# Kernel optimization log

Measured on AMD Instinct MI355X. Metric: run time of the kernel, lower is better.

Reference implementation:

```python
import jax, jax.numpy as jnp
import numpy as np

B, S, D, H, HD = 1, 2048, 1024, 16, 64
E, K, F = 8, 2, 2048
Z_COEF, LB_COEF = 0.001, 0.01


def setup_inputs() -> dict:
    key = jax.random.key(0)
    ks = jax.random.split(key, 10)
    s_d = 1.0 / np.sqrt(D)
    s_f = 1.0 / np.sqrt(F)
    return {
        'hidden_states': jax.random.normal(ks[0], (B, S, D), jnp.float32),
        'attention_mask': jnp.tril(jnp.ones((S, S), bool))[None, None],  # causal [1,1,S,S]
        'position_ids': jnp.broadcast_to(jnp.arange(S), (B, S)),
        'ln1_w': jnp.ones((D,), jnp.float32), 'ln1_b': jnp.zeros((D,), jnp.float32),
        'ln2_w': jnp.ones((D,), jnp.float32), 'ln2_b': jnp.zeros((D,), jnp.float32),
        'wq': jax.random.normal(ks[1], (D, D), jnp.float32) * s_d,
        'wk': jax.random.normal(ks[2], (D, D), jnp.float32) * s_d,
        'wv': jax.random.normal(ks[3], (D, D), jnp.float32) * s_d,
        'wo': jax.random.normal(ks[4], (D, D), jnp.float32) * s_d,
        'w_router': jax.random.normal(ks[5], (D, E), jnp.float32) * s_d,
        'w_gate': jax.random.normal(ks[6], (E, D, F), jnp.float32) * s_d,
        'w_up': jax.random.normal(ks[7], (E, D, F), jnp.float32) * s_d,
        'w_down': jax.random.normal(ks[8], (E, F, D), jnp.float32) * s_f,
    }


def _layernorm(x, w, b):
    m = x.mean(-1, keepdims=True)
    v = jnp.mean(jnp.square(x - m), -1, keepdims=True)
    return (x - m) / jnp.sqrt(v + 1e-5) * w + b


def _rotate_half(x):
    x1, x2 = jnp.split(x, 2, axis=-1)
    return jnp.concatenate([-x2, x1], axis=-1)


def _forward(hs, mask, pos, l1w, l1b, l2w, l2b, wq, wk, wv, wo, wr, wg, wu, wd):
    b, s, d = hs.shape
    # --- attention sub-block ---
    res = hs
    x = _layernorm(hs, l1w, l1b)
    q = (x @ wq).reshape(b, s, H, HD).transpose(0, 2, 1, 3)  # [b,H,s,hd]
    k = (x @ wk).reshape(b, s, H, HD).transpose(0, 2, 1, 3)
    v = (x @ wv).reshape(b, s, H, HD).transpose(0, 2, 1, 3)
    inv_freq = 1.0 / (10000.0 ** (jnp.arange(0, HD, 2, dtype=jnp.float32) / HD))
    freqs = pos[..., None].astype(jnp.float32) * inv_freq  # [b,s,hd/2]
    cos = jnp.cos(freqs); sin = jnp.sin(freqs)
    cos = jnp.concatenate([cos, cos], -1)[:, None]  # [b,1,s,hd]
    sin = jnp.concatenate([sin, sin], -1)[:, None]
    q = q * cos + _rotate_half(q) * sin
    k = k * cos + _rotate_half(k) * sin
    scores = jnp.einsum('bhqd,bhkd->bhqk', q, k) / np.sqrt(HD)
    scores = jnp.where(mask, scores, jnp.asarray(-1e9, scores.dtype))
    attn_w = jax.nn.softmax(scores, axis=-1)
    a = jnp.einsum('bhqk,bhkd->bhqd', attn_w, v)
    a = a.transpose(0, 2, 1, 3).reshape(b, s, d)
    hs = res + a @ wo
    # --- MoE sub-block ---
    res = hs
    x = _layernorm(hs, l2w, l2b)
    xt = x.reshape(-1, d)  # [T,D]
    logits = xt @ wr  # [T,E]
    probs = jax.nn.softmax(logits.astype(jnp.float32), axis=-1)
    ew, ei = jax.lax.top_k(probs, K)  # [T,K]
    ew = ew / ew.sum(-1, keepdims=True)
    one_hot = jax.nn.one_hot(ei, E, dtype=jnp.float32)  # [T,K,E]
    combine = jnp.sum(one_hot * ew[..., None], axis=1).astype(xt.dtype)  # [T,E]
    g = jnp.einsum('td,edf->etf', xt, wg)
    u = jnp.einsum('td,edf->etf', xt, wu)
    y = jnp.einsum('etf,efd->etd', jax.nn.silu(g) * u, wd)  # [E,T,D]
    moe_out = jnp.einsum('te,etd->td', combine, y).reshape(b, s, d)
    # --- aux losses ---
    z_loss = Z_COEF * jnp.mean(jnp.square(jax.scipy.special.logsumexp(logits, axis=-1)))
    expert_mask = jnp.sum(one_hot, axis=1)  # [T,E] in {0,1}
    util = expert_mask.sum(0) / (b * s)
    lb_loss = LB_COEF * jnp.sum(util * probs.mean(0))
    aux = z_loss + lb_loss
    return res + moe_out, aux


def reference(hidden_states, attention_mask, position_ids, ln1_w, ln1_b, ln2_w, ln2_b,
              wq, wk, wv, wo, w_router, w_gate, w_up, w_down):
    return _forward(hidden_states, attention_mask, position_ids, ln1_w, ln1_b, ln2_w, ln2_b,
                    wq, wk, wv, wo, w_router, w_gate, w_up, w_down)
```

## Files before the change

kernel.cpp:

```cpp
#include <hip/hip_runtime.h>
#include <math.h>

static constexpr int S = 2048;
static constexpr int D = 1024;
static constexpr int H = 16;
static constexpr int HD = 64;
static constexpr int E = 8;
static constexpr int F = 2048;
static constexpr int NSLOTS = S * 2;
static constexpr int NPAD = NSLOTS + 128;

typedef __attribute__((ext_vector_type(8))) short bf16x8;
typedef __attribute__((ext_vector_type(4))) float f32x4;

__device__ __forceinline__ float bf2f(ushort u) {
    uint32_t x = ((uint32_t)u) << 16; float f; __builtin_memcpy(&f, &x, 4); return f;
}
__device__ __forceinline__ ushort f2bf(float f) {
    uint32_t x; __builtin_memcpy(&x, &f, 4);
    return (ushort)((x + 0x7fffu + ((x >> 16) & 1u)) >> 16);
}
__device__ __forceinline__ void async_copy16(const void* gptr, void* ldsptr) {
    __builtin_amdgcn_global_load_lds(
        (const __attribute__((address_space(1))) void*)gptr,
        (__attribute__((address_space(3))) void*)ldsptr, 16, 0, 0);
}

__global__ __launch_bounds__(256) void castT_kernel(const float* __restrict__ src,
    ushort* __restrict__ dst, int K, int N)
{
    __shared__ float T[64][65];
    int z = blockIdx.z;
    src += (size_t)z * K * N; dst += (size_t)z * K * N;
    int k0 = blockIdx.y * 64, n0 = blockIdx.x * 64;
    int t = threadIdx.x;
    int r = t >> 4, c4 = (t & 15) * 4;
#pragma unroll
    for (int it = 0; it < 4; it++) {
        float4 v = *(const float4*)(src + (size_t)(k0 + r + it * 16) * N + n0 + c4);
        T[r + it * 16][c4 + 0] = v.x; T[r + it * 16][c4 + 1] = v.y;
        T[r + it * 16][c4 + 2] = v.z; T[r + it * 16][c4 + 3] = v.w;
    }
    __syncthreads();
#pragma unroll
    for (int it = 0; it < 4; it++) {
        int rr = r + it * 16;
        ushort4 o;
        o.x = f2bf(T[c4 + 0][rr]); o.y = f2bf(T[c4 + 1][rr]);
        o.z = f2bf(T[c4 + 2][rr]); o.w = f2bf(T[c4 + 3][rr]);
        *(ushort4*)(dst + (size_t)(n0 + rr) * K + k0 + c4) = o;
    }
}

__global__ __launch_bounds__(256) void castT2_kernel(const float* __restrict__ src,
    ushort* __restrict__ dh, ushort* __restrict__ dl, int K, int N)
{
    __shared__ float T[64][65];
    src += (size_t)blockIdx.z * K * N;
    dh += (size_t)blockIdx.z * K * N; dl += (size_t)blockIdx.z * K * N;
    int k0 = blockIdx.y * 64, n0 = blockIdx.x * 64;
    int t = threadIdx.x;
    int r = t >> 4, c4 = (t & 15) * 4;
#pragma unroll
    for (int it = 0; it < 4; it++) {
        float4 v = *(const float4*)(src + (size_t)(k0 + r + it * 16) * N + n0 + c4);
        T[r + it * 16][c4 + 0] = v.x; T[r + it * 16][c4 + 1] = v.y;
        T[r + it * 16][c4 + 2] = v.z; T[r + it * 16][c4 + 3] = v.w;
    }
    __syncthreads();
#pragma unroll
    for (int it = 0; it < 4; it++) {
        int rr = r + it * 16;
        ushort4 oh, ol;
        float v0 = T[c4 + 0][rr], v1 = T[c4 + 1][rr], v2 = T[c4 + 2][rr], v3 = T[c4 + 3][rr];
        oh.x = f2bf(v0); ol.x = f2bf(v0 - bf2f(oh.x));
        oh.y = f2bf(v1); ol.y = f2bf(v1 - bf2f(oh.y));
        oh.z = f2bf(v2); ol.z = f2bf(v2 - bf2f(oh.z));
        oh.w = f2bf(v3); ol.w = f2bf(v3 - bf2f(oh.w));
        *(ushort4*)(dh + (size_t)(n0 + rr) * K + k0 + c4) = oh;
        *(ushort4*)(dl + (size_t)(n0 + rr) * K + k0 + c4) = ol;
    }
}

__global__ __launch_bounds__(256) void ln_kernel(const float* __restrict__ x,
    const float* __restrict__ w, const float* __restrict__ b,
    float* __restrict__ yf, ushort* __restrict__ yh, ushort* __restrict__ yl)
{
    int t = blockIdx.x, tid = threadIdx.x;
    __shared__ float redx[256];
    __shared__ float redy[256];
    const float* xr = x + (size_t)t * D;
    float4 xv = *(const float4*)(xr + tid * 4);
    redx[tid] = xv.x + xv.y + xv.z + xv.w;
    redy[tid] = xv.x * xv.x + xv.y * xv.y + xv.z * xv.z + xv.w * xv.w;
    __syncthreads();
    for (int st = 128; st > 0; st >>= 1) {
        if (tid < st) { redx[tid] += redx[tid + st]; redy[tid] += redy[tid + st]; }
        __syncthreads();
    }
    float mean = redx[0] * (1.0f / D);
    float var  = redy[0] * (1.0f / D) - mean * mean;
    float rstd = rsqrtf(var + 1e-5f);
    float4 wv = *(const float4*)(w + tid * 4);
    float4 bv = *(const float4*)(b + tid * 4);
    float4 o;
    o.x = (xv.x - mean) * rstd * wv.x + bv.x;
    o.y = (xv.y - mean) * rstd * wv.y + bv.y;
    o.z = (xv.z - mean) * rstd * wv.z + bv.z;
    o.w = (xv.w - mean) * rstd * wv.w + bv.w;
    if (yf) *(float4*)(yf + (size_t)t * D + tid * 4) = o;
    ushort4 oh;
    oh.x = f2bf(o.x); oh.y = f2bf(o.y); oh.z = f2bf(o.z); oh.w = f2bf(o.w);
    if (yh) *(ushort4*)(yh + (size_t)t * D + tid * 4) = oh;
    if (yl) {
        ushort4 ol;
        ol.x = f2bf(o.x - bf2f(oh.x)); ol.y = f2bf(o.y - bf2f(oh.y));
        ol.z = f2bf(o.z - bf2f(oh.z)); ol.w = f2bf(o.w - bf2f(oh.w));
        *(ushort4*)(yl + (size_t)t * D + tid * 4) = ol;
    }
}

__global__ __launch_bounds__(512) void rope_cast(const float* __restrict__ q,
    const float* __restrict__ k, ushort* __restrict__ qh, ushort* __restrict__ ql,
    ushort* __restrict__ kh, ushort* __restrict__ kl)
{
    int t = blockIdx.x;
    int idx = threadIdx.x;
    int hh = idx >> 5, i = idx & 31;
    float invf = powf(10000.0f, -(float)i / 32.0f);
    float ang = (float)t * invf;
    float cc = cosf(ang), ss = sinf(ang);
    size_t base = (size_t)t * D + hh * HD + i;
    const float QS = 0.125f * 1.4426950408889634f;
    float q1 = q[base], q2 = q[base + 32];
    float qr1 = (q1 * cc - q2 * ss) * QS;
    float qr2 = (q2 * cc + q1 * ss) * QS;
    ushort h1 = f2bf(qr1); qh[base] = h1;      ql[base] = f2bf(qr1 - bf2f(h1));
    ushort h2 = f2bf(qr2); qh[base + 32] = h2; ql[base + 32] = f2bf(qr2 - bf2f(h2));
    float k1 = k[base], k2 = k[base + 32];
    float kr1 = k1 * cc - k2 * ss;
    float kr2 = k2 * cc + k1 * ss;
    ushort h3 = f2bf(kr1); kh[base] = h3;      kl[base] = f2bf(kr1 - bf2f(h3));
    ushort h4 = f2bf(kr2); kh[base + 32] = h4; kl[base + 32] = f2bf(kr2 - bf2f(h4));
}

__device__ __forceinline__ void stage_m2(const ushort* __restrict__ Ah_g,
    const ushort* __restrict__ Al_g, const ushort* __restrict__ Bh_g,
    const ushort* __restrict__ Bl_g, int lda, int ldb, int kbase,
    ushort* sAh, ushort* sAl, ushort* sBh, ushort* sBl, int tid, int w)
{
    {
        int ckc = tid >> 6, r = tid & 63;
        int loff = (w * 64) * 8;
        size_t ga = (size_t)r * lda + kbase + ckc * 8;
        async_copy16(Ah_g + ga, sAh + loff);
        async_copy16(Al_g + ga, sAl + loff);
    }
#pragma unroll
    for (int it = 0; it < 2; it++) {
        int c = it * 256 + tid;
        int ckc = c >> 7, r = c & 127;
        int loff = (it * 256 + w * 64) * 8;
        size_t gb = (size_t)r * ldb + kbase + ckc * 8;
        async_copy16(Bh_g + gb, sBh + loff);
        async_copy16(Bl_g + gb, sBl + loff);
    }
}

__device__ __forceinline__ void mfma2_kloop(const ushort* __restrict__ Ah_g,
    const ushort* __restrict__ Al_g, const ushort* __restrict__ Bh_g,
    const ushort* __restrict__ Bl_g, int lda, int ldb, int K,
    ushort (&sAh)[2][2048], ushort (&sAl)[2][2048],
    ushort (&sBh)[2][4096], ushort (&sBl)[2][4096], f32x4 (&acc)[2][4])
{
    const int tid = threadIdx.x;
    const int w = tid >> 6, l = tid & 63;
    const int wm = (w >> 1) * 32, wn = (w & 1) * 64;
    const int kc = l >> 4, lr = l & 15;
    const int NT = K / 32;
    stage_m2(Ah_g, Al_g, Bh_g, Bl_g, lda, ldb, 0, sAh[0], sAl[0], sBh[0], sBl[0], tid, w);
    for (int t = 0; t < NT; ++t) {
        const int cur = t & 1;
        asm volatile("s_waitcnt vmcnt(0)" ::: "memory");
        __builtin_amdgcn_s_barrier();
        __builtin_amdgcn_sched_barrier(0);
        if (t + 1 < NT)
            stage_m2(Ah_g, Al_g, Bh_g, Bl_g, lda, ldb, (t + 1) * 32,
                     sAh[1 - cur], sAl[1 - cur], sBh[1 - cur], sBl[1 - cur], tid, w);
        bf16x8 ah[2], al[2], bh[4], bl[4];
#pragma unroll
        for (int f = 0; f < 2; f++) {
            int ao = (kc * 64 + wm + f * 16 + lr) * 8;
            ah[f] = *(const bf16x8*)(sAh[cur] + ao);
            al[f] = *(const bf16x8*)(sAl[cur] + ao);
        }
#pragma unroll
        for (int f = 0; f < 4; f++) {
            int bo = (kc * 128 + wn + f * 16 + lr) * 8;
            bh[f] = *(const bf16x8*)(sBh[cur] + bo);
            bl[f] = *(const bf16x8*)(sBl[cur] + bo);
        }
#pragma unroll
        for (int fm = 0; fm < 2; fm++)
#pragma unroll
            for (int fn = 0; fn < 4; fn++) {
                acc[fm][fn] = __builtin_amdgcn_mfma_f32_16x16x32_bf16(ah[fm], bh[fn], acc[fm][fn], 0, 0, 0);
                acc[fm][fn] = __builtin_amdgcn_mfma_f32_16x16x32_bf16(ah[fm], bl[fn], acc[fm][fn], 0, 0, 0);
                acc[fm][fn] = __builtin_amdgcn_mfma_f32_16x16x32_bf16(al[fm], bh[fn], acc[fm][fn], 0, 0, 0);
            }
    }
}

__global__ __launch_bounds__(256) void qkv_mfma2(const ushort* __restrict__ xh,
    const ushort* __restrict__ xl,
    const ushort* __restrict__ wqh, const ushort* __restrict__ wql,
    const ushort* __restrict__ wkh, const ushort* __restrict__ wkl,
    const ushort* __restrict__ wvh, const ushort* __restrict__ wvl,
    float* __restrict__ qo, float* __restrict__ ko, float* __restrict__ vo)
{
    __shared__ ushort sAh[2][2048], sAl[2][2048], sBh[2][4096], sBl[2][4096];
    const ushort* Bh = blockIdx.z == 0 ? wqh : (blockIdx.z == 1 ? wkh : wvh);
    const ushort* Bl = blockIdx.z == 0 ? wql : (blockIdx.z == 1 ? wkl : wvl);
    float* C = blockIdx.z == 0 ? qo : (blockIdx.z == 1 ? ko : vo);
    int m0 = blockIdx.y * 64, n0 = blockIdx.x * 128;
    f32x4 acc[2][4];
#pragma unroll
    for (int i = 0; i < 2; i++)
#pragma unroll
        for (int j = 0; j < 4; j++) acc[i][j] = (f32x4){0.f, 0.f, 0.f, 0.f};
    mfma2_kloop(xh + (size_t)m0 * D, xl + (size_t)m0 * D,
                Bh + (size_t)n0 * D, Bl + (size_t)n0 * D, D, D, D,
                sAh, sAl, sBh, sBl, acc);
    const int l = threadIdx.x & 63, w = threadIdx.x >> 6;
    const int wm = (w >> 1) * 32, wn = (w & 1) * 64;
#pragma unroll
    for (int fm = 0; fm < 2; fm++)
#pragma unroll
        for (int fn = 0; fn < 4; fn++)
#pragma unroll
            for (int r = 0; r < 4; r++) {
                int row = m0 + wm + fm * 16 + (l >> 4) * 4 + r;
                int col = n0 + wn + fn * 16 + (l & 15);
                C[(size_t)row * D + col] = acc[fm][fn][r];
            }
}

__global__ __launch_bounds__(256) void wo_mfma2(const ushort* __restrict__ ah,
    const ushort* __restrict__ al, const ushort* __restrict__ wh, const ushort* __restrict__ wl,
    const float* __restrict__ resid, float* __restrict__ Cout)
{
    __shared__ ushort sAh[2][2048], sAl[2][2048], sBh[2][4096], sBl[2][4096];
    int m0 = blockIdx.y * 64, n0 = blockIdx.x * 128;
    f32x4 acc[2][4];
#pragma unroll
    for (int i = 0; i < 2; i++)
#pragma unroll
        for (int j = 0; j < 4; j++) acc[i][j] = (f32x4){0.f, 0.f, 0.f, 0.f};
    mfma2_kloop(ah + (size_t)m0 * D, al + (size_t)m0 * D,
                wh + (size_t)n0 * D, wl + (size_t)n0 * D, D, D, D,
                sAh, sAl, sBh, sBl, acc);
    const int l = threadIdx.x & 63, w = threadIdx.x >> 6;
    const int wm = (w >> 1) * 32, wn = (w & 1) * 64;
#pragma unroll
    for (int fm = 0; fm < 2; fm++)
#pragma unroll
        for (int fn = 0; fn < 4; fn++)
#pragma unroll
            for (int r = 0; r < 4; r++) {
                int row = m0 + wm + fm * 16 + (l >> 4) * 4 + r;
                int col = n0 + wn + fn * 16 + (l & 15);
                Cout[(size_t)row * D + col] = acc[fm][fn][r] + resid[(size_t)row * D + col];
            }
}

__global__ __launch_bounds__(256) void attn_mfma(
    const ushort* __restrict__ qhp, const ushort* __restrict__ qlp,
    const ushort* __restrict__ khp, const ushort* __restrict__ klp,
    const ushort* __restrict__ vth, const ushort* __restrict__ vtl,
    ushort* __restrict__ oh_out, ushort* __restrict__ ol_out)
{
    __shared__ ushort sK[2][2][4096];
    __shared__ ushort sV[2][2][4096];
    __shared__ ushort sP[4][2][1024];
    const int n = blockIdx.y * 32 + blockIdx.x;
    const int wg = ((n & 7) << 6) + (n >> 3);
    const int h = wg >> 5;
    const int qt = 31 - (wg & 31);
    const int tid = threadIdx.x;
    const int w = tid >> 6, l = tid & 63;
    const int g = l >> 4, c = l & 15;
    const size_t hoff = (size_t)h * HD;
    ushort* sPh = &sP[w][0][0];
    ushort* sPl = &sP[w][1][0];

#define STAGE_KV(buf, kt_)                                                        \
  do {                                                                            \
    const int k0s = (kt_) * 64;                                                   \
    int cb0 = w * 64;                                                             \
    int ch0 = cb0 + l;                                                            \
    size_t kg0 = (size_t)(k0s + (ch0 & 63)) * D + hoff + (ch0 >> 6) * 8;          \
    size_t vg0 = (hoff + (ch0 & 63)) * (size_t)S + k0s + (ch0 >> 6) * 8;          \
    async_copy16(khp + kg0, &sK[buf][0][cb0 * 8]);                                \
    async_copy16(klp + kg0, &sK[buf][1][cb0 * 8]);                                \
    async_copy16(vth + vg0, &sV[buf][0][cb0 * 8]);                                \
    async_copy16(vtl + vg0, &sV[buf][1][cb0 * 8]);                                \
    int cb1 = 256 + w * 64;                                                       \
    int ch1 = cb1 + l;                                                            \
    size_t kg1 = (size_t)(k0s + (ch1 & 63)) * D + hoff + (ch1 >> 6) * 8;          \
    size_t vg1 = (hoff + (ch1 & 63)) * (size_t)S + k0s + (ch1 >> 6) * 8;          \
    async_copy16(khp + kg1, &sK[buf][0][cb1 * 8]);                                \
    async_copy16(klp + kg1, &sK[buf][1][cb1 * 8]);                                \
    async_copy16(vth + vg1, &sV[buf][0][cb1 * 8]);                                \
// ... 90 lines not shown
        }
        const ushort* sVh = &sV[cur][0][0];
        const ushort* sVl = &sV[cur][1][0];
        bf16x8 pa0 = *(const bf16x8*)(sPh + (g * 16 + c) * 8);
        bf16x8 pa1 = *(const bf16x8*)(sPh + ((4 + g) * 16 + c) * 8);
        bf16x8 pb0 = *(const bf16x8*)(sPl + (g * 16 + c) * 8);
        bf16x8 pb1 = *(const bf16x8*)(sPl + ((4 + g) * 16 + c) * 8);
#pragma unroll
        for (int fn = 0; fn < 4; fn++) {
            int u0 = (g * 64 + fn * 16 + c) * 8;
            int u1 = ((4 + g) * 64 + fn * 16 + c) * 8;
            bf16x8 vh0 = *(const bf16x8*)(sVh + u0);
            bf16x8 vh1 = *(const bf16x8*)(sVh + u1);
            bf16x8 vl0 = *(const bf16x8*)(sVl + u0);
            bf16x8 vl1 = *(const bf16x8*)(sVl + u1);
            f32x4 o = oacc[fn];
            o = __builtin_amdgcn_mfma_f32_16x16x32_bf16(pa0, vh0, o, 0, 0, 0);
            o = __builtin_amdgcn_mfma_f32_16x16x32_bf16(pa1, vh1, o, 0, 0, 0);
            o = __builtin_amdgcn_mfma_f32_16x16x32_bf16(pa0, vl0, o, 0, 0, 0);
            o = __builtin_amdgcn_mfma_f32_16x16x32_bf16(pa1, vl1, o, 0, 0, 0);
            o = __builtin_amdgcn_mfma_f32_16x16x32_bf16(pb0, vh0, o, 0, 0, 0);
            o = __builtin_amdgcn_mfma_f32_16x16x32_bf16(pb1, vh1, o, 0, 0, 0);
            oacc[fn] = o;
        }
        if (kt < qt) {
            asm volatile("s_waitcnt vmcnt(0)" ::: "memory");
            __builtin_amdgcn_s_barrier();
            __builtin_amdgcn_sched_barrier(0);
        }
    }
#pragma unroll
    for (int r = 0; r < 4; r++) {
        float inv = 1.0f / l_[r];
        size_t orow = (size_t)(qt * 64 + w * 16 + g * 4 + r) * D + hoff;
#pragma unroll
        for (int fn = 0; fn < 4; fn++) {
            float v = oacc[fn][r] * inv;
            ushort hi = f2bf(v);
            oh_out[orow + fn * 16 + c] = hi;
            ol_out[orow + fn * 16 + c] = f2bf(v - bf2f(hi));
        }
    }
#undef STAGE_KV
}

__global__ __launch_bounds__(64) void router_kernel(const float* __restrict__ x,
    const float* __restrict__ wr, int* __restrict__ ei, float* __restrict__ ew,
    int* __restrict__ counts, float* __restrict__ prob_sums, float* __restrict__ z_sum)
{
    int t = blockIdx.x, lane = threadIdx.x;
    const float* xr = x + (size_t)t * D;
    float p[E] = {};
    for (int d = lane; d < D; d += 64) {
        float xd = xr[d];
        const float* wrow = wr + d * E;
#pragma unroll
        for (int e = 0; e < E; e++) p[e] = fmaf(xd, wrow[e], p[e]);
    }
#pragma unroll
    for (int off = 32; off > 0; off >>= 1) {
#pragma unroll
        for (int e = 0; e < E; e++) p[e] += __shfl_xor(p[e], off);
    }
    float m = p[0];
#pragma unroll
    for (int e = 1; e < E; e++) m = fmaxf(m, p[e]);
    float sum = 0.0f, pr[E];
#pragma unroll
    for (int e = 0; e < E; e++) { pr[e] = expf(p[e] - m); sum += pr[e]; }
    float invs = 1.0f / sum;
#pragma unroll
    for (int e = 0; e < E; e++) pr[e] *= invs;
    float lse = m + logf(sum);
// ... 20 lines not shown
    if (tid < E) { counts[tid] = 0; prob_sums[tid] = 0.0f; }
    if (tid == 0) *z_sum = 0.0f;
}

__global__ void finalize_kernel(const int* __restrict__ counts, const float* __restrict__ prob_sums,
    const float* __restrict__ z_sum, int* __restrict__ offs, int* __restrict__ cursor,
    float* __restrict__ aux_out)
{
    if (threadIdx.x == 0) {
        int off = 0;
        for (int e = 0; e < E; e++) { offs[e] = off; cursor[e] = off; off += counts[e]; }
        float z = 1e-3f * (*z_sum) * (1.0f / S);
        float lb = 0.0f;
        for (int e = 0; e < E; e++) lb += ((float)counts[e] / (float)S) * (prob_sums[e] / (float)S);
        lb *= 1e-2f;
        *aux_out = z + lb;
    }
}

__global__ __launch_bounds__(256) void scatter_kernel(const int* __restrict__ ei,
    int* __restrict__ cursor, int* __restrict__ tlist, int* __restrict__ slot_of)
{
    int t = blockIdx.x * 256 + threadIdx.x;
    if (t >= S) return;
#pragma unroll
    for (int kk = 0; kk < 2; kk++) {
        int e = ei[2 * t + kk];
        int slot = atomicAdd(&cursor[e], 1);
        tlist[slot] = t;
        slot_of[2 * t + kk] = slot;
    }
}

__global__ __launch_bounds__(256) void gather_kernel(const ushort* __restrict__ xbf,
    const int* __restrict__ tlist, ushort* __restrict__ xg)
{
    int slot = blockIdx.x;
    int t4 = threadIdx.x * 4;
    ushort4 vv;
    if (slot < NSLOTS) {
        int tok = tlist[slot];
        vv = *(const ushort4*)(xbf + (size_t)tok * D + t4);
    } else {
        vv = make_ushort4(0, 0, 0, 0);
    }
    *(ushort4*)(xg + (size_t)slot * D + t4) = vv;
}

__global__ __launch_bounds__(256) void moe_gateup_mfma(const ushort* __restrict__ xg,
    const ushort* __restrict__ wgt, const ushort* __restrict__ wut,
    ushort* __restrict__ Hg, ushort* __restrict__ Hu,
    const int* __restrict__ offs, const int* __restrict__ cnts)
{
    const int e = blockIdx.z;
    const int cnt = cnts[e];
    const int m0 = blockIdx.y * 64;
    if (m0 >= cnt) return;
    const int off = offs[e];
    const int n0g = blockIdx.x * 128;
    const bool isg = n0g < F;
    const ushort* Wt = isg ? (wgt + (size_t)e * F * D + (size_t)n0g * D)
                           : (wut + (size_t)e * F * D + (size_t)(n0g - F) * D);
    ushort* Outp = isg ? Hg : Hu;
    const int ncol0 = isg ? n0g : n0g - F;
    __shared__ ushort As[3][2048], Ws[3][4096];
    const int tid = threadIdx.x;
    const int w = tid >> 6, l = tid & 63;
    const int wm = (w >> 1) * 32, wn = (w & 1) * 64;
    const int kc = l >> 4, lr = l & 15;
    const ushort* Arow = xg + (size_t)(off + m0) * D;

#define STAGE_GU(buf, t_)                                                     \
  do {                                                                        \
    int kbase = (t_) * 32;                                                    \
    {                                                                         \
      int ckc = tid >> 6, r = tid & 63;                                       \
      int loff = (w * 64) * 8;                                                \
      async_copy16(Arow + (size_t)r * D + kbase + ckc * 8, As[buf] + loff);   \
    }                                                                         \
    _Pragma("unroll")                                                         \
    for (int it = 0; it < 2; it++) {                                          \
      int cch = it * 256 + tid;                                               \
      int ckc = cch >> 7, r = cch & 127;                                      \
      int loff = (it * 256 + w * 64) * 8;                                     \
      async_copy16(Wt + (size_t)r * D + kbase + ckc * 8, Ws[buf] + loff);     \
    }                                                                         \
  } while (0)

    f32x4 acc[2][4];
#pragma unroll
    for (int i = 0; i < 2; i++)
#pragma unroll
        for (int j = 0; j < 4; j++) acc[i][j] = (f32x4){0.f, 0.f, 0.f, 0.f};

    const int NT = D / 32;
    STAGE_GU(0, 0);
    STAGE_GU(1, 1);
    for (int t = 0; t < NT; ++t) {
        const int cur = t % 3;
        if (t + 1 < NT) { asm volatile("s_waitcnt vmcnt(3)" ::: "memory"); }
        else            { asm volatile("s_waitcnt vmcnt(0)" ::: "memory"); }
        __builtin_amdgcn_s_barrier();
        __builtin_amdgcn_sched_barrier(0);
        if (t + 2 < NT) STAGE_GU((t + 2) % 3, t + 2);
        bf16x8 af[2], wf[4];
#pragma unroll
        for (int f = 0; f < 2; f++)
            af[f] = *(const bf16x8*)(As[cur] + (kc * 64 + wm + f * 16 + lr) * 8);
#pragma unroll
        for (int f = 0; f < 4; f++)
            wf[f] = *(const bf16x8*)(Ws[cur] + (kc * 128 + wn + f * 16 + lr) * 8);
#pragma unroll
        for (int fm = 0; fm < 2; fm++)
#pragma unroll
            for (int fn = 0; fn < 4; fn++)
                acc[fm][fn] = __builtin_amdgcn_mfma_f32_16x16x32_bf16(af[fm], wf[fn], acc[fm][fn], 0, 0, 0);
    }
#undef STAGE_GU
#pragma unroll
    for (int fm = 0; fm < 2; fm++)
#pragma unroll
        for (int fn = 0; fn < 4; fn++)
#pragma unroll
            for (int r = 0; r < 4; r++) {
                int rloc = m0 + wm + fm * 16 + (l >> 4) * 4 + r;
                if (rloc < cnt) {
                    int col = ncol0 + wn + fn * 16 + (l & 15);
                    Outp[(size_t)(off + rloc) * F + col] = f2bf(acc[fm][fn][r]);
                }
            }
}

__global__ __launch_bounds__(256) void silu_kernel(const ushort* __restrict__ Gout,
    const ushort* __restrict__ Uout, ushort* __restrict__ Hb)
{
    int slot = blockIdx.x;
    int f0 = threadIdx.x * 8;
    bf16x8 gv = *(const bf16x8*)(Gout + (size_t)slot * F + f0);
    bf16x8 uv = *(const bf16x8*)(Uout + (size_t)slot * F + f0);
    bf16x8 o;
#pragma unroll
    for (int j = 0; j < 8; j++) {
        float g = bf2f((ushort)gv[j]);
        float u = bf2f((ushort)uv[j]);
        o[j] = (short)f2bf(g / (1.0f + expf(-g)) * u);
    }
    *(bf16x8*)(Hb + (size_t)slot * F + f0) = o;
}

__global__ __launch_bounds__(256) void moe_down_mfma(const ushort* __restrict__ Hb,
    const ushort* __restrict__ wdt, ushort* __restrict__ yb,
    const int* __restrict__ offs, const int* __restrict__ cnts)
{
    const int e = blockIdx.z;
    const int cnt = cnts[e];
    const int m0 = blockIdx.y * 64;
    if (m0 >= cnt) return;
    const int off = offs[e];
    const ushort* Bt = wdt + (size_t)e * D * F;
    const int n0 = blockIdx.x * 128;
    __shared__ ushort As[3][2048], Bs[3][4096];
    const int tid = threadIdx.x;
    const int w = tid >> 6, l = tid & 63;
    const int wm = (w >> 1) * 32, wn = (w & 1) * 64;
    const int kc = l >> 4, lr = l & 15;
    const ushort* Arow = Hb + (size_t)(off + m0) * F;
    const ushort* Brow = Bt + (size_t)n0 * F;

#define STAGE_DN(buf, t_)                                                     \
  do {                                                                        \
    int kbase = (t_) * 32;                                                    \
    {                                                                         \
      int ckc = tid >> 6, r = tid & 63;                                       \
      int loff = (w * 64) * 8;                                                \
      async_copy16(Arow + (size_t)r * F + kbase + ckc * 8, As[buf] + loff);   \
    }                                                                         \
    _Pragma("unroll")                                                         \
    for (int it = 0; it < 2; it++) {                                          \
      int cch = it * 256 + tid;                                               \
      int ckc = cch >> 7, r = cch & 127;                                      \
      int loff = (it * 256 + w * 64) * 8;                                     \
      async_copy16(Brow + (size_t)r * F + kbase + ckc * 8, Bs[buf] + loff);   \
    }                                                                         \
  } while (0)

    f32x4 acc[2][4];
#pragma unroll
    for (int i = 0; i < 2; i++)
#pragma unroll
        for (int j = 0; j < 4; j++) acc[i][j] = (f32x4){0.f,0.f,0.f,0.f};

    const int NT = F / 32;
    STAGE_DN(0, 0);
    STAGE_DN(1, 1);
    for (int t = 0; t < NT; ++t) {
        const int cur = t % 3;
        if (t + 1 < NT) { asm volatile("s_waitcnt vmcnt(3)" ::: "memory"); }
        else            { asm volatile("s_waitcnt vmcnt(0)" ::: "memory"); }
        __builtin_amdgcn_s_barrier();
        __builtin_amdgcn_sched_barrier(0);
        if (t + 2 < NT) STAGE_DN((t + 2) % 3, t + 2);
        bf16x8 af[2], bfr[4];
#pragma unroll
        for (int f = 0; f < 2; f++)
            af[f] = *(const bf16x8*)(As[cur] + (kc * 64 + wm + f * 16 + lr) * 8);
#pragma unroll
        for (int f = 0; f < 4; f++)
            bfr[f] = *(const bf16x8*)(Bs[cur] + (kc * 128 + wn + f * 16 + lr) * 8);
#pragma unroll
        for (int fm = 0; fm < 2; fm++)
#pragma unroll
            for (int fn = 0; fn < 4; fn++)
                acc[fm][fn] = __builtin_amdgcn_mfma_f32_16x16x32_bf16(af[fm], bfr[fn], acc[fm][fn], 0, 0, 0);
    }
#undef STAGE_DN
#pragma unroll
    for (int fm = 0; fm < 2; fm++)
// ... 62 lines not shown
    ushort* wvlo = (ushort*)alloc((size_t)D * D * 2);
    ushort* woh  = (ushort*)alloc((size_t)D * D * 2);
    ushort* wolo = (ushort*)alloc((size_t)D * D * 2);
    ushort* xh   = (ushort*)alloc(TD * 2);
    ushort* xl   = (ushort*)alloc(TD * 2);
    float*  qb   = (float*)alloc(TD * 4);
    float*  kb   = (float*)alloc(TD * 4);
    float*  vb   = (float*)alloc(TD * 4);
    ushort* ath  = (ushort*)alloc(TD * 2);
    ushort* atl  = (ushort*)alloc(TD * 2);
    float*  hs2  = (float*)alloc(TD * 4);
    float*  xf32 = (float*)alloc(TD * 4);
    ushort* xbf  = (ushort*)alloc(TD * 2);
    ushort* xg   = (ushort*)alloc((size_t)NPAD * D * 2);
    ushort* Hb   = (ushort*)alloc((size_t)NPAD * F * 2);
    ushort* yb   = (ushort*)alloc((size_t)NPAD * D * 2);
    ushort* khp  = (ushort*)alloc(TD * 2);
    ushort* klp  = (ushort*)alloc(TD * 2);
    ushort* vth  = (ushort*)alloc(TD * 2);
    ushort* vtl  = (ushort*)alloc(TD * 2);
    float*  ewb       = (float*)alloc(2 * S * 4);
    float*  prob_sums = (float*)alloc(8 * 4);
    float*  z_sum     = (float*)alloc(8 * 4);
    int* ei      = (int*)alloc(2 * S * 4);
    int* slot_of = (int*)alloc(2 * S * 4);
    int* tlist   = (int*)alloc(NSLOTS * 4);
    int* counts  = (int*)alloc(8 * 4);
    int* offs    = (int*)alloc(8 * 4);
    int* cursor  = (int*)alloc(8 * 4);

    ushort* Gout = (ushort*)qb;
    ushort* Uout = (ushort*)vb;

    castT2_kernel<<<dim3(D / 64, D / 64, 1), 256, 0, stream>>>(wq, wqh, wqlo, D, D);
    castT2_kernel<<<dim3(D / 64, D / 64, 1), 256, 0, stream>>>(wk, wkh, wklo, D, D);
    castT2_kernel<<<dim3(D / 64, D / 64, 1), 256, 0, stream>>>(wv, wvh, wvlo, D, D);
    castT2_kernel<<<dim3(D / 64, D / 64, 1), 256, 0, stream>>>(wo, woh, wolo, D, D);
    castT_kernel<<<dim3(F / 64, D / 64, E), 256, 0, stream>>>(wg, wgt, D, F);
    castT_kernel<<<dim3(F / 64, D / 64, E), 256, 0, stream>>>(wu, wut, D, F);
    castT_kernel<<<dim3(D / 64, F / 64, E), 256, 0, stream>>>(wd, wdt, F, D);

    ln_kernel<<<S, 256, 0, stream>>>(hs, ln1w, ln1b, nullptr, xh, xl);
    qkv_mfma2<<<dim3(D / 128, S / 64, 3), 256, 0, stream>>>(xh, xl, wqh, wqlo, wkh, wklo, wvh, wvlo, qb, kb, vb);
    rope_cast<<<S, 512, 0, stream>>>(qb, kb, xh, xl, khp, klp);
    castT2_kernel<<<dim3(D / 64, S / 64, 1), 256, 0, stream>>>(vb, vth, vtl, S, D);
    attn_mfma<<<dim3(32, 16), 256, 0, stream>>>(xh, xl, khp, klp, vth, vtl, ath, atl);
    wo_mfma2<<<dim3(D / 128, S / 64), 256, 0, stream>>>(ath, atl, woh, wolo, hs, hs2);

    ln_kernel<<<S, 256, 0, stream>>>(hs2, ln2w, ln2b, xf32, xbf, nullptr);
    zero_kernel<<<1, 64, 0, stream>>>(counts, prob_sums, z_sum);
    router_kernel<<<S, 64, 0, stream>>>(xf32, wr, ei, ewb, counts, prob_sums, z_sum);
    finalize_kernel<<<1, 64, 0, stream>>>(counts, prob_sums, z_sum, offs, cursor, out + TD);
    scatter_kernel<<<S / 256, 256, 0, stream>>>(ei, cursor, tlist, slot_of);
    gather_kernel<<<NPAD, 256, 0, stream>>>(xbf, tlist, xg);
    moe_gateup_mfma<<<dim3(2 * F / 128, NSLOTS / 64, E), 256, 0, stream>>>(xg, wgt, wut, Gout, Uout, offs, counts);
    silu_kernel<<<NSLOTS, 256, 0, stream>>>(Gout, Uout, Hb);
    moe_down_mfma<<<dim3(D / 128, NSLOTS / 64, E), 256, 0, stream>>>(Hb, wdt, yb, offs, counts);
    combine_kernel<<<S, 256, 0, stream>>>(hs2, yb, ewb, slot_of, out);
}
```

Measured before the change: 862.1 us.

## Pre-tile GEMM operands into LDS-ready contiguous tile layouts

Weight casts, LayerNorm output, the attention output, the MoE gather and the SiLU output now write their bf16 data straight into a blocked tile layout that matches the GEMMs' LDS staging order. The QKV, Wo, gate/up and down GEMMs then stage each k-step with fully contiguous 16-byte-per-lane async copies instead of strided row reads. This is meant to improve global-load coalescing and simplify address math in the GEMM main loops. In exchange, the producer kernels do scattered, less coalesced writes, and the layout indexing is spread across many kernels, which makes it fragile.

Measured after the change: 748.8 us. 1.15x faster.

```diff
diff --git a/kernel.cpp b/kernel.cpp
--- a/kernel.cpp
+++ b/kernel.cpp
@@ -26,29 +26,65 @@
         (__attribute__((address_space(3))) void*)ldsptr, 16, 0, 0);
 }
 
-__global__ __launch_bounds__(256) void castT_kernel(const float* __restrict__ src,
+__global__ __launch_bounds__(256) void castTileW_kernel(const float* __restrict__ src,
     ushort* __restrict__ dst, int K, int N)
 {
-    __shared__ float T[64][65];
-    int z = blockIdx.z;
-    src += (size_t)z * K * N; dst += (size_t)z * K * N;
-    int k0 = blockIdx.y * 64, n0 = blockIdx.x * 64;
-    int t = threadIdx.x;
-    int r = t >> 4, c4 = (t & 15) * 4;
-#pragma unroll
-    for (int it = 0; it < 4; it++) {
-        float4 v = *(const float4*)(src + (size_t)(k0 + r + it * 16) * N + n0 + c4);
-        T[r + it * 16][c4 + 0] = v.x; T[r + it * 16][c4 + 1] = v.y;
-        T[r + it * 16][c4 + 2] = v.z; T[r + it * 16][c4 + 3] = v.w;
+    __shared__ float T[32][132];
+    src += (size_t)blockIdx.z * K * N;
+    dst += (size_t)blockIdx.z * K * N;
+    const int p = blockIdx.x, t = blockIdx.y;
+    const int tid = threadIdx.x;
+    const int k = tid >> 3, nb = (tid & 7) * 16;
+    const float* sr = src + (size_t)(t * 32 + k) * N + p * 128 + nb;
+#pragma unroll
+    for (int q = 0; q < 4; q++) {
+        float4 v = *(const float4*)(sr + q * 4);
+        T[k][nb + q * 4 + 0] = v.x; T[k][nb + q * 4 + 1] = v.y;
+        T[k][nb + q * 4 + 2] = v.z; T[k][nb + q * 4 + 3] = v.w;
     }
     __syncthreads();
-#pragma unroll
-    for (int it = 0; it < 4; it++) {
-        int rr = r + it * 16;
-        ushort4 o;
-        o.x = f2bf(T[c4 + 0][rr]); o.y = f2bf(T[c4 + 1][rr]);
-        o.z = f2bf(T[c4 + 2][rr]); o.w = f2bf(T[c4 + 3][rr]);
-        *(ushort4*)(dst + (size_t)(n0 + rr) * K + k0 + c4) = o;
+    ushort* dbase = dst + ((size_t)p * (K / 32) + t) * 4096;
+#pragma unroll
+    for (int q = 0; q < 2; q++) {
+        int c = tid * 2 + q;
+        int kc = c >> 7, n = c & 127;
+        bf16x8 o;
+#pragma unroll
+        for (int j = 0; j < 8; j++) o[j] = (short)f2bf(T[kc * 8 + j][n]);
+        *(bf16x8*)(dbase + (size_t)c * 8) = o;
+    }
+}
+
+__global__ __launch_bounds__(256) void castTile2W_kernel(const float* __restrict__ src,
+    ushort* __restrict__ dh, ushort* __restrict__ dl, int K, int N)
+{
+    __shared__ float T[32][132];
+    const int p = blockIdx.x, t = blockIdx.y;
+    const int tid = threadIdx.x;
+    const int k = tid >> 3, nb = (tid & 7) * 16;
+    const float* sr = src + (size_t)(t * 32 + k) * N + p * 128 + nb;
+#pragma unroll
+    for (int q = 0; q < 4; q++) {
+        float4 v = *(const float4*)(sr + q * 4);
+        T[k][nb + q * 4 + 0] = v.x; T[k][nb + q * 4 + 1] = v.y;
+        T[k][nb + q * 4 + 2] = v.z; T[k][nb + q * 4 + 3] = v.w;
+    }
+    __syncthreads();
+    size_t tb = ((size_t)p * (K / 32) + t) * 4096;
+#pragma unroll
+    for (int q = 0; q < 2; q++) {
+        int c = tid * 2 + q;
+        int kc = c >> 7, n = c & 127;
+        bf16x8 oh, ol;
+#pragma unroll
+        for (int j = 0; j < 8; j++) {
+            float v = T[kc * 8 + j][n];
+            ushort h = f2bf(v);
+            oh[j] = (short)h;
+            ol[j] = (short)f2bf(v - bf2f(h));
+        }
+        *(bf16x8*)(dh + tb + (size_t)c * 8) = oh;
+        *(bf16x8*)(dl + tb + (size_t)c * 8) = ol;
     }
 }
 
@@ -56,8 +92,6 @@
     ushort* __restrict__ dh, ushort* __restrict__ dl, int K, int N)
 {
     __shared__ float T[64][65];
-    src += (size_t)blockIdx.z * K * N;
-    dh += (size_t)blockIdx.z * K * N; dl += (size_t)blockIdx.z * K * N;
     int k0 = blockIdx.y * 64, n0 = blockIdx.x * 64;
     int t = threadIdx.x;
     int r = t >> 4, c4 = (t & 15) * 4;
@@ -84,12 +118,13 @@
 
 __global__ __launch_bounds__(256) void ln_kernel(const float* __restrict__ x,
     const float* __restrict__ w, const float* __restrict__ b,
-    float* __restrict__ yf, ushort* __restrict__ yh, ushort* __restrict__ yl)
-{
-    int t = blockIdx.x, tid = threadIdx.x;
+    float* __restrict__ yf, ushort* __restrict__ yh,
+    ushort* __restrict__ th, ushort* __restrict__ tl)
+{
+    int tk = blockIdx.x, tid = threadIdx.x;
     __shared__ float redx[256];
     __shared__ float redy[256];
-    const float* xr = x + (size_t)t * D;
+    const float* xr = x + (size_t)tk * D;
     float4 xv = *(const float4*)(xr + tid * 4);
     redx[tid] = xv.x + xv.y + xv.z + xv.w;
     redy[tid] = xv.x * xv.x + xv.y * xv.y + xv.z * xv.z + xv.w * xv.w;
@@ -108,15 +143,19 @@
     o.y = (xv.y - mean) * rstd * wv.y + bv.y;
     o.z = (xv.z - mean) * rstd * wv.z + bv.z;
     o.w = (xv.w - mean) * rstd * wv.w + bv.w;
-    if (yf) *(float4*)(yf + (size_t)t * D + tid * 4) = o;
+    if (yf) *(float4*)(yf + (size_t)tk * D + tid * 4) = o;
     ushort4 oh;
     oh.x = f2bf(o.x); oh.y = f2bf(o.y); oh.z = f2bf(o.z); oh.w = f2bf(o.w);
-    if (yh) *(ushort4*)(yh + (size_t)t * D + tid * 4) = oh;
-    if (yl) {
+    if (yh) *(ushort4*)(yh + (size_t)tk * D + tid * 4) = oh;
+    if (th) {
+        int d0 = tid * 4;
+        size_t ta = (((size_t)(tk >> 6) * 32 + (d0 >> 5)) * 256
+                     + (size_t)((d0 >> 3) & 3) * 64 + (tk & 63)) * 8 + (d0 & 7);
+        *(ushort4*)(th + ta) = oh;
         ushort4 ol;
         ol.x = f2bf(o.x - bf2f(oh.x)); ol.y = f2bf(o.y - bf2f(oh.y));
         ol.z = f2bf(o.z - bf2f(oh.z)); ol.w = f2bf(o.w - bf2f(oh.w));
-        *(ushort4*)(yl + (size_t)t * D + tid * 4) = ol;
+        *(ushort4*)(tl + ta) = ol;
     }
 }
 
@@ -144,32 +183,22 @@
     ushort h4 = f2bf(kr2); kh[base + 32] = h4; kl[base + 32] = f2bf(kr2 - bf2f(h4));
 }
 
-__device__ __forceinline__ void stage_m2(const ushort* __restrict__ Ah_g,
-    const ushort* __restrict__ Al_g, const ushort* __restrict__ Bh_g,
-    const ushort* __restrict__ Bl_g, int lda, int ldb, int kbase,
+__device__ __forceinline__ void stage_t2(const ushort* __restrict__ Ath, const ushort* __restrict__ Atl,
+    const ushort* __restrict__ Bth, const ushort* __restrict__ Btl, size_t abase, size_t bbase,
     ushort* sAh, ushort* sAl, ushort* sBh, ushort* sBl, int tid, int w)
 {
-    {
-        int ckc = tid >> 6, r = tid & 63;
-        int loff = (w * 64) * 8;
-        size_t ga = (size_t)r * lda + kbase + ckc * 8;
-        async_copy16(Ah_g + ga, sAh + loff);
-        async_copy16(Al_g + ga, sAl + loff);
-    }
-#pragma unroll
-    for (int it = 0; it < 2; it++) {
-        int c = it * 256 + tid;
-        int ckc = c >> 7, r = c & 127;
-        int loff = (it * 256 + w * 64) * 8;
-        size_t gb = (size_t)r * ldb + kbase + ckc * 8;
-        async_copy16(Bh_g + gb, sBh + loff);
-        async_copy16(Bl_g + gb, sBl + loff);
-    }
-}
-
-__device__ __forceinline__ void mfma2_kloop(const ushort* __restrict__ Ah_g,
-    const ushort* __restrict__ Al_g, const ushort* __restrict__ Bh_g,
-    const ushort* __restrict__ Bl_g, int lda, int ldb, int K,
+    const int wo8 = w * 512;
+    async_copy16(Ath + abase + (size_t)tid * 8, sAh + wo8);
+    async_copy16(Atl + abase + (size_t)tid * 8, sAl + wo8);
+    async_copy16(Bth + bbase + (size_t)tid * 8, sBh + wo8);
+    async_copy16(Btl + bbase + (size_t)tid * 8, sBl + wo8);
+    async_copy16(Bth + bbase + (size_t)(256 + tid) * 8, sBh + 2048 + wo8);
+    async_copy16(Btl + bbase + (size_t)(256 + tid) * 8, sBl + 2048 + wo8);
+}
+
+__device__ __forceinline__ void mfma2_kloop_t(const ushort* __restrict__ Ath,
+    const ushort* __restrict__ Atl, const ushort* __restrict__ Bth, const ushort* __restrict__ Btl,
+    int KT, int mt,
     ushort (&sAh)[2][2048], ushort (&sAl)[2][2048],
     ushort (&sBh)[2][4096], ushort (&sBl)[2][4096], f32x4 (&acc)[2][4])
 {
@@ -177,15 +206,15 @@
     const int w = tid >> 6, l = tid & 63;
     const int wm = (w >> 1) * 32, wn = (w & 1) * 64;
     const int kc = l >> 4, lr = l & 15;
-    const int NT = K / 32;
-    stage_m2(Ah_g, Al_g, Bh_g, Bl_g, lda, ldb, 0, sAh[0], sAl[0], sBh[0], sBl[0], tid, w);
-    for (int t = 0; t < NT; ++t) {
+    const size_t a0 = (size_t)mt * KT * 2048;
+    stage_t2(Ath, Atl, Bth, Btl, a0, 0, sAh[0], sAl[0], sBh[0], sBl[0], tid, w);
+    for (int t = 0; t < KT; ++t) {
         const int cur = t & 1;
         asm volatile("s_waitcnt vmcnt(0)" ::: "memory");
         __builtin_amdgcn_s_barrier();
         __builtin_amdgcn_sched_barrier(0);
-        if (t + 1 < NT)
-            stage_m2(Ah_g, Al_g, Bh_g, Bl_g, lda, ldb, (t + 1) * 32,
+        if (t + 1 < KT)
+            stage_t2(Ath, Atl, Bth, Btl, a0 + (size_t)(t + 1) * 2048, (size_t)(t + 1) * 4096,
                      sAh[1 - cur], sAl[1 - cur], sBh[1 - cur], sBl[1 - cur], tid, w);
         bf16x8 ah[2], al[2], bh[4], bl[4];
 #pragma unroll
@@ -222,15 +251,15 @@
     const ushort* Bh = blockIdx.z == 0 ? wqh : (blockIdx.z == 1 ? wkh : wvh);
     const ushort* Bl = blockIdx.z == 0 ? wql : (blockIdx.z == 1 ? wkl : wvl);
     float* C = blockIdx.z == 0 ? qo : (blockIdx.z == 1 ? ko : vo);
-    int m0 = blockIdx.y * 64, n0 = blockIdx.x * 128;
+    int mt = blockIdx.y, ntile = blockIdx.x;
+    int m0 = mt * 64, n0 = ntile * 128;
     f32x4 acc[2][4];
 #pragma unroll
     for (int i = 0; i < 2; i++)
 #pragma unroll
         for (int j = 0; j < 4; j++) acc[i][j] = (f32x4){0.f, 0.f, 0.f, 0.f};
-    mfma2_kloop(xh + (size_t)m0 * D, xl + (size_t)m0 * D,
-                Bh + (size_t)n0 * D, Bl + (size_t)n0 * D, D, D, D,
-                sAh, sAl, sBh, sBl, acc);
+    mfma2_kloop_t(xh, xl, Bh + (size_t)ntile * 32 * 4096, Bl + (size_t)ntile * 32 * 4096,
+                  32, mt, sAh, sAl, sBh, sBl, acc);
     const int l = threadIdx.x & 63, w = threadIdx.x >> 6;
     const int wm = (w >> 1) * 32, wn = (w & 1) * 64;
 #pragma unroll
@@ -245,20 +274,20 @@
             }
 }
 
-__global__ __launch_bounds__(256) void wo_mfma2(const ushort* __restrict__ ah,
-    const ushort* __restrict__ al, const ushort* __restrict__ wh, const ushort* __restrict__ wl,
+__global__ __launch_bounds__(256) void wo_mfma2(const ushort* __restrict__ aht,
+    const ushort* __restrict__ alt, const ushort* __restrict__ wh, const ushort* __restrict__ wl,
     const float* __restrict__ resid, float* __restrict__ Cout)
 {
     __shared__ ushort sAh[2][2048], sAl[2][2048], sBh[2][4096], sBl[2][4096];
-    int m0 = blockIdx.y * 64, n0 = blockIdx.x * 128;
+    int mt = blockIdx.y, ntile = blockIdx.x;
+    int m0 = mt * 64, n0 = ntile * 128;
     f32x4 acc[2][4];
 #pragma unroll
     for (int i = 0; i < 2; i++)
 #pragma unroll
         for (int j = 0; j < 4; j++) acc[i][j] = (f32x4){0.f, 0.f, 0.f, 0.f};
-    mfma2_kloop(ah + (size_t)m0 * D, al + (size_t)m0 * D,
-                wh + (size_t)n0 * D, wl + (size_t)n0 * D, D, D, D,
-                sAh, sAl, sBh, sBl, acc);
+    mfma2_kloop_t(aht, alt, wh + (size_t)ntile * 32 * 4096, wl + (size_t)ntile * 32 * 4096,
+                  32, mt, sAh, sAl, sBh, sBl, acc);
     const int l = threadIdx.x & 63, w = threadIdx.x >> 6;
     const int wm = (w >> 1) * 32, wn = (w & 1) * 64;
 #pragma unroll
@@ -277,7 +306,7 @@
     const ushort* __restrict__ qhp, const ushort* __restrict__ qlp,
     const ushort* __restrict__ khp, const ushort* __restrict__ klp,
     const ushort* __restrict__ vth, const ushort* __restrict__ vtl,
-    ushort* __restrict__ oh_out, ushort* __restrict__ ol_out)
+    ushort* __restrict__ aht, ushort* __restrict__ alt)
 {
     __shared__ ushort sK[2][2][4096];
     __shared__ ushort sV[2][2][4096];
@@ -434,13 +463,15 @@
 #pragma unroll
     for (int r = 0; r < 4; r++) {
         float inv = 1.0f / l_[r];
-        size_t orow = (size_t)(qt * 64 + w * 16 + g * 4 + r) * D + hoff;
+        int rowin = w * 16 + g * 4 + r;
 #pragma unroll
         for (int fn = 0; fn < 4; fn++) {
             float v = oacc[fn][r] * inv;
             ushort hi = f2bf(v);
-            oh_out[orow + fn * 16 + c] = hi;
-            ol_out[orow + fn * 16 + c] = f2bf(v - bf2f(hi));
+            size_t ta = (((size_t)qt * 32 + h * 2 + (fn >> 1)) * 256
+                         + (size_t)((fn * 2 + (c >> 3)) & 3) * 64 + rowin) * 8 + (c & 7);
+            aht[ta] = hi;
+            alt[ta] = f2bf(v - bf2f(hi));
         }
     }
 #undef STAGE_KV
@@ -527,23 +558,25 @@
     }
 }
 
-__global__ __launch_bounds__(256) void gather_kernel(const ushort* __restrict__ xbf,
-    const int* __restrict__ tlist, ushort* __restrict__ xg)
+__global__ __launch_bounds__(128) void gather_kernel(const ushort* __restrict__ xbf,
+    const int* __restrict__ tlist, ushort* __restrict__ xgT)
 {
     int slot = blockIdx.x;
-    int t4 = threadIdx.x * 4;
-    ushort4 vv;
+    int tid = threadIdx.x;
+    bf16x8 v;
     if (slot < NSLOTS) {
         int tok = tlist[slot];
-        vv = *(const ushort4*)(xbf + (size_t)tok * D + t4);
+        v = *(const bf16x8*)(xbf + (size_t)tok * D + tid * 8);
     } else {
-        vv = make_ushort4(0, 0, 0, 0);
-    }
-    *(ushort4*)(xg + (size_t)slot * D + t4) = vv;
-}
-
-__global__ __launch_bounds__(256) void moe_gateup_mfma(const ushort* __restrict__ xg,
-    const ushort* __restrict__ wgt, const ushort* __restrict__ wut,
+        v = (bf16x8){0, 0, 0, 0, 0, 0, 0, 0};
+    }
+    size_t addr = (((size_t)(slot >> 6) * 32 + (tid >> 2)) * 256
+                   + (size_t)(tid & 3) * 64 + (slot & 63)) * 8;
+    *(bf16x8*)(xgT + addr) = v;
+}
+
+__global__ __launch_bounds__(256) void moe_gateup_mfma(const ushort* __restrict__ xgT,
+    const ushort* __restrict__ wgT, const ushort* __restrict__ wuT,
     ushort* __restrict__ Hg, ushort* __restrict__ Hu,
     const int* __restrict__ offs, const int* __restrict__ cnts)
 {
@@ -554,8 +587,8 @@
     const int off = offs[e];
     const int n0g = blockIdx.x * 128;
     const bool isg = n0g < F;
-    const ushort* Wt = isg ? (wgt + (size_t)e * F * D + (size_t)n0g * D)
-                           : (wut + (size_t)e * F * D + (size_t)(n0g - F) * D);
+    const int p = isg ? (n0g >> 7) : ((n0g - F) >> 7);
+    const ushort* Wt = (isg ? wgT : wuT) + (size_t)e * F * D + (size_t)p * 32 * 4096;
     ushort* Outp = isg ? Hg : Hu;
     const int ncol0 = isg ? n0g : n0g - F;
     __shared__ ushort As[3][2048], Ws[3][4096];
@@ -563,24 +596,15 @@
     const int w = tid >> 6, l = tid & 63;
     const int wm = (w >> 1) * 32, wn = (w & 1) * 64;
     const int kc = l >> 4, lr = l & 15;
-    const ushort* Arow = xg + (size_t)(off + m0) * D;
-
-#define STAGE_GU(buf, t_)                                                     \
-  do {                                                                        \
-    int kbase = (t_) * 32;                                                    \
-    {                                                                         \
-      int ckc = tid >> 6, r = tid & 63;                                       \
-      int loff = (w * 64) * 8;                                                \
-      async_copy16(Arow + (size_t)r * D + kbase + ckc * 8, As[buf] + loff);   \
-    }                                                                         \
-    _Pragma("unroll")                                                         \
-    for (int it = 0; it < 2; it++) {                                          \
-      int cch = it * 256 + tid;                                               \
-      int ckc = cch >> 7, r = cch & 127;                                      \
-      int loff = (it * 256 + w * 64) * 8;                                     \
-      async_copy16(Wt + (size_t)r * D + kbase + ckc * 8, Ws[buf] + loff);     \
-    }                                                                         \
-  } while (0)
+    const int wo8 = w * 512;
+    const int sl = off + m0 + l;
+    const size_t A0 = (size_t)(sl >> 6) * 65536 + ((size_t)w * 64 + (sl & 63)) * 8;
+
+#define STAGE_GU(buf, t_) do {                                                    \
+    async_copy16(xgT + A0 + (size_t)(t_) * 2048, As[buf] + wo8);                  \
+    async_copy16(Wt + (size_t)(t_) * 4096 + (size_t)tid * 8, Ws[buf] + wo8);      \
+    async_copy16(Wt + (size_t)(t_) * 4096 + (size_t)(256 + tid) * 8, Ws[buf] + 2048 + wo8); \
+} while (0)
 
     f32x4 acc[2][4];
 #pragma unroll
@@ -627,10 +651,11 @@
 }
 
 __global__ __launch_bounds__(256) void silu_kernel(const ushort* __restrict__ Gout,
-    const ushort* __restrict__ Uout, ushort* __restrict__ Hb)
+    const ushort* __restrict__ Uout, ushort* __restrict__ HbT)
 {
     int slot = blockIdx.x;
-    int f0 = threadIdx.x * 8;
+    int tid = threadIdx.x;
+    int f0 = tid * 8;
     bf16x8 gv = *(const bf16x8*)(Gout + (size_t)slot * F + f0);
     bf16x8 uv = *(const bf16x8*)(Uout + (size_t)slot * F + f0);
     bf16x8 o;
@@ -640,11 +665,13 @@
         float u = bf2f((ushort)uv[j]);
         o[j] = (short)f2bf(g / (1.0f + expf(-g)) * u);
     }
-    *(bf16x8*)(Hb + (size_t)slot * F + f0) = o;
-}
-
-__global__ __launch_bounds__(256) void moe_down_mfma(const ushort* __restrict__ Hb,
-    const ushort* __restrict__ wdt, ushort* __restrict__ yb,
+    size_t addr = (((size_t)(slot >> 6) * 64 + (tid >> 2)) * 256
+                   + (size_t)(tid & 3) * 64 + (slot & 63)) * 8;
+    *(bf16x8*)(HbT + addr) = o;
+}
+
+__global__ __launch_bounds__(256) void moe_down_mfma(const ushort* __restrict__ HbT,
+    const ushort* __restrict__ wdT, ushort* __restrict__ yb,
     const int* __restrict__ offs, const int* __restrict__ cnts)
 {
     const int e = blockIdx.z;
@@ -652,32 +679,23 @@
     const int m0 = blockIdx.y * 64;
     if (m0 >= cnt) return;
     const int off = offs[e];
-    const ushort* Bt = wdt + (size_t)e * D * F;
-    const int n0 = blockIdx.x * 128;
+    const int p = blockIdx.x;
+    const int n0 = p * 128;
+    const ushort* Wt = wdT + (size_t)e * D * F + (size_t)p * 64 * 4096;
     __shared__ ushort As[3][2048], Bs[3][4096];
     const int tid = threadIdx.x;
     const int w = tid >> 6, l = tid & 63;
     const int wm = (w >> 1) * 32, wn = (w & 1) * 64;
     const int kc = l >> 4, lr = l & 15;
-    const ushort* Arow = Hb + (size_t)(off + m0) * F;
-    const ushort* Brow = Bt + (size_t)n0 * F;
-
-#define STAGE_DN(buf, t_)                                                     \
-  do {                                                                        \
-    int kbase = (t_) * 32;                                                    \
-    {                                                                         \
-      int ckc = tid >> 6, r = tid & 63;                                       \
-      int loff = (w * 64) * 8;                                                \
-      async_copy16(Arow + (size_t)r * F + kbase + ckc * 8, As[buf] + loff);   \
-    }                                                                         \
-    _Pragma("unroll")                                                         \
-    for (int it = 0; it < 2; it++) {                                          \
-      int cch = it * 256 + tid;                                               \
-      int ckc = cch >> 7, r = cch & 127;                                      \
-      int loff = (it * 256 + w * 64) * 8;                                     \
-      async_copy16(Brow + (size_t)r * F + kbase + ckc * 8, Bs[buf] + loff);   \
-    }                                                                         \
-  } while (0)
+    const int wo8 = w * 512;
+    const int sl = off + m0 + l;
+    const size_t A0 = (size_t)(sl >> 6) * 131072 + ((size_t)w * 64 + (sl & 63)) * 8;
+
+#define STAGE_DN(buf, t_) do {                                                    \
+    async_copy16(HbT + A0 + (size_t)(t_) * 2048, As[buf] + wo8);                  \
+    async_copy16(Wt + (size_t)(t_) * 4096 + (size_t)tid * 8, Bs[buf] + wo8);      \
+    async_copy16(Wt + (size_t)(t_) * 4096 + (size_t)(256 + tid) * 8, Bs[buf] + 2048 + wo8); \
+} while (0)
 
     f32x4 acc[2][4];
 #pragma unroll
@@ -806,27 +824,27 @@
     ushort* Gout = (ushort*)qb;
     ushort* Uout = (ushort*)vb;
 
-    castT2_kernel<<<dim3(D / 64, D / 64, 1), 256, 0, stream>>>(wq, wqh, wqlo, D, D);
-    castT2_kernel<<<dim3(D / 64, D / 64, 1), 256, 0, stream>>>(wk, wkh, wklo, D, D);
-    castT2_kernel<<<dim3(D / 64, D / 64, 1), 256, 0, stream>>>(wv, wvh, wvlo, D, D);
-    castT2_kernel<<<dim3(D / 64, D / 64, 1), 256, 0, stream>>>(wo, woh, wolo, D, D);
-    castT_kernel<<<dim3(F / 64, D / 64, E), 256, 0, stream>>>(wg, wgt, D, F);
-    castT_kernel<<<dim3(F / 64, D / 64, E), 256, 0, stream>>>(wu, wut, D, F);
-    castT_kernel<<<dim3(D / 64, F / 64, E), 256, 0, stream>>>(wd, wdt, F, D);
-
-    ln_kernel<<<S, 256, 0, stream>>>(hs, ln1w, ln1b, nullptr, xh, xl);
+    castTile2W_kernel<<<dim3(D / 128, D / 32), 256, 0, stream>>>(wq, wqh, wqlo, D, D);
+    castTile2W_kernel<<<dim3(D / 128, D / 32), 256, 0, stream>>>(wk, wkh, wklo, D, D);
+    castTile2W_kernel<<<dim3(D / 128, D / 32), 256, 0, stream>>>(wv, wvh, wvlo, D, D);
+    castTile2W_kernel<<<dim3(D / 128, D / 32), 256, 0, stream>>>(wo, woh, wolo, D, D);
+    castTileW_kernel<<<dim3(F / 128, D / 32, E), 256, 0, stream>>>(wg, wgt, D, F);
+    castTileW_kernel<<<dim3(F / 128, D / 32, E), 256, 0, stream>>>(wu, wut, D, F);
+    castTileW_kernel<<<dim3(D / 128, F / 32, E), 256, 0, stream>>>(wd, wdt, F, D);
+
+    ln_kernel<<<S, 256, 0, stream>>>(hs, ln1w, ln1b, nullptr, nullptr, xh, xl);
     qkv_mfma2<<<dim3(D / 128, S / 64, 3), 256, 0, stream>>>(xh, xl, wqh, wqlo, wkh, wklo, wvh, wvlo, qb, kb, vb);
     rope_cast<<<S, 512, 0, stream>>>(qb, kb, xh, xl, khp, klp);
-    castT2_kernel<<<dim3(D / 64, S / 64, 1), 256, 0, stream>>>(vb, vth, vtl, S, D);
+    castT2_kernel<<<dim3(D / 64, S / 64), 256, 0, stream>>>(vb, vth, vtl, S, D);
     attn_mfma<<<dim3(32, 16), 256, 0, stream>>>(xh, xl, khp, klp, vth, vtl, ath, atl);
     wo_mfma2<<<dim3(D / 128, S / 64), 256, 0, stream>>>(ath, atl, woh, wolo, hs, hs2);
 
-    ln_kernel<<<S, 256, 0, stream>>>(hs2, ln2w, ln2b, xf32, xbf, nullptr);
+    ln_kernel<<<S, 256, 0, stream>>>(hs2, ln2w, ln2b, xf32, xbf, nullptr, nullptr);
     zero_kernel<<<1, 64, 0, stream>>>(counts, prob_sums, z_sum);
     router_kernel<<<S, 64, 0, stream>>>(xf32, wr, ei, ewb, counts, prob_sums, z_sum);
     finalize_kernel<<<1, 64, 0, stream>>>(counts, prob_sums, z_sum, offs, cursor, out + TD);
     scatter_kernel<<<S / 256, 256, 0, stream>>>(ei, cursor, tlist, slot_of);
-    gather_kernel<<<NPAD, 256, 0, stream>>>(xbf, tlist, xg);
+    gather_kernel<<<NPAD, 128, 0, stream>>>(xbf, tlist, xg);
     moe_gateup_mfma<<<dim3(2 * F / 128, NSLOTS / 64, E), 256, 0, stream>>>(xg, wgt, wut, Gout, Uout, offs, counts);
     silu_kernel<<<NSLOTS, 256, 0, stream>>>(Gout, Uout, Hb);
     moe_down_mfma<<<dim3(D / 128, NSLOTS / 64, E), 256, 0, stream>>>(Hb, wdt, yb, offs, counts);
```
